# Performance work log

Hardware: AMD Instinct MI355X
Metric: run time of the kernel (lower is better)

The kernel has to match this reference:

```python
import jax, jax.numpy as jnp
import numpy as np

D_MODEL = 256
D_INNER = 512   # expand * d_model
NHEADS = 8
HEADDIM = 64    # d_inner // nheads
NGROUPS = 1
MDIST = 16


def setup_inputs() -> dict:
    key = jax.random.key(0)
    ks = jax.random.split(key, 12)
    B, L, Q = 4, 2048, 300
    in_key = jax.random.normal(ks[0], (B, L, D_MODEL), jnp.float32)
    in_query = jax.random.normal(ks[1], (B, Q, D_MODEL), jnp.float32)
    dist = jax.random.normal(ks[2], (B, L, Q, MDIST), jnp.float32)

    def lin(k, out_f, in_f):  # torch nn.Linear default init (kaiming-uniform-ish)
        bound = 1.0 / np.sqrt(in_f)
        return jax.random.uniform(k, (out_f, in_f), jnp.float32, -bound, bound)

    W_key = lin(ks[3], 2 * D_INNER + 2 * NGROUPS + NHEADS, D_MODEL)
    W_query = lin(ks[4], D_INNER, D_MODEL)
    W_bc = lin(ks[5], 2 * NGROUPS, MDIST)
    W_dt = lin(ks[6], NHEADS, MDIST)
    # dt_bias init (inverse-softplus of dt sampled log-uniform in [1e-4, 0.1])
    dt_min, dt_max = 1e-4, 0.1
    dtv = jnp.exp(jax.random.uniform(ks[7], (NHEADS,)) * (np.log(dt_max) - np.log(dt_min)) + np.log(dt_min))
    dtv = jnp.clip(dtv, 1e-4, None)
    dt_bias = dtv + jnp.log(-jnp.expm1(-dtv))
    A_log = jnp.log(jax.random.uniform(ks[8], (NHEADS,), minval=1.0, maxval=16.0))
    Dp = jnp.ones((NHEADS,), jnp.float32)
    W_out_key = lin(ks[9], D_MODEL, D_INNER)
    W_out_query = lin(ks[10], D_MODEL, D_INNER)
    key_norm_w = jnp.ones((D_INNER,), jnp.float32)
    ln_w = jnp.ones((D_INNER,), jnp.float32)
    ln_b = jnp.zeros((D_INNER,), jnp.float32)
    return dict(in_key=in_key, in_query=in_query, dist=dist, W_key=W_key, W_query=W_query,
                W_bc=W_bc, W_dt=W_dt, dt_bias=dt_bias, A_log=A_log, Dp=Dp,
                W_out_key=W_out_key, W_out_query=W_out_query, key_norm_w=key_norm_w,
                ln_w=ln_w, ln_b=ln_b)


def _issm_scan(x, S0, dt, A, Bm, Cm, Dp):
    """Selective scan with per-(l,h,n) dt and per-(l,n) B,C (ngroups=1).
    x: (B,L,H,P)  dt: (B,L,H,N)  Bm,Cm: (B,L,N)  S0: (B,H,P,N)  A: (H,)  Dp: (H,)
    """
    xs = (jnp.moveaxis(x, 1, 0), jnp.moveaxis(dt, 1, 0),
          jnp.moveaxis(Bm, 1, 0), jnp.moveaxis(Cm, 1, 0))

    def step(S, inp):
        xl, dtl, Bl, Cl = inp               # (B,H,P), (B,H,N), (B,N), (B,N)
        dA = jnp.exp(dtl * A[None, :, None])            # (B,H,N)
        dBx = (dtl * Bl[:, None, :])[:, :, None, :] * xl[:, :, :, None]
        S = S * dA[:, :, None, :] + dBx                 # (B,H,P,N)
        y = jnp.einsum('bhpn,bn->bhp', S, Cl) + Dp[None, :, None] * xl
        return S, y

    Sf, ys = jax.lax.scan(step, S0, xs)
    return jnp.moveaxis(ys, 0, 1), Sf       # (B,L,H,P), (B,H,P,N)


def reference(in_key, in_query, dist, W_key, W_query, W_bc, W_dt, dt_bias, A_log, Dp,
              W_out_key, W_out_query, key_norm_w, ln_w, ln_b):
    B, L, _ = in_key.shape
    Q = in_query.shape[1]
    zxbcdt = in_key @ W_key.T                            # (B,L,2*Din+2g+H)
    z = zxbcdt[..., :D_INNER]
    x = zxbcdt[..., D_INNER:2 * D_INNER].reshape(B, L, NHEADS, HEADDIM)
    b_bias = zxbcdt[..., 2 * D_INNER:2 * D_INNER + 1]    # (B,L,1)
    c_bias = zxbcdt[..., 2 * D_INNER + 1:2 * D_INNER + 2]
    dt_proj_bias = zxbcdt[..., 2 * D_INNER + 2:]         # (B,L,H)

    # initial state: (B,H,P,Q) -- state dim N == num_queries
    S0 = (in_query @ W_query.T).reshape(B, Q, NHEADS, HEADDIM).transpose(0, 2, 3, 1)
    A = -jnp.exp(A_log)                                  # (H,), constant over state dim

    bc = jnp.einsum('blqm,cm->blqc', dist, W_bc)         # (B,L,Q,2)
    Bm = bc[..., 0] + b_bias                             # (B,L,Q)
    Cm = bc[..., 1] + c_bias
    dtb = jnp.einsum('blqm,hm->blhq', dist, W_dt)        # (B,L,H,Q)
    dt = jax.nn.softplus(dtb + dt_proj_bias[..., None] + dt_bias[None, None, :, None])

    y_f, S_f = _issm_scan(x, S0, dt, A, Bm, Cm, Dp)
    # bidirectional: backward branch uses identical (cloned) x/B/C, flipped along L
    y_b, S_b = _issm_scan(x[:, ::-1], S0, dt[:, ::-1], A, Bm[:, ::-1], Cm[:, ::-1], Dp)
    y = (y_f + y_b[:, ::-1]) * 0.5
    S = (S_f + S_b) * 0.5

    key = y.reshape(B, L, D_INNER)
    g = key * jax.nn.silu(z)                             # gated RMSNorm, norm_before_gate=False
    key = g * jax.lax.rsqrt(jnp.mean(g * g, -1, keepdims=True) + 1e-5) * key_norm_w
    out_key = key @ W_out_key.T

    ls = S.transpose(0, 3, 1, 2).reshape(B, Q, D_INNER)  # b h p q -> b q (h p)
    mu = jnp.mean(ls, -1, keepdims=True)
    var = jnp.mean((ls - mu) ** 2, -1, keepdims=True)
    ls = (ls - mu) * jax.lax.rsqrt(var + 1e-5) * ln_w + ln_b
    out_query = ls @ W_out_query.T
    return out_key, out_query
```

## Files before the change

kernel.cpp:

```cpp
#include <hip/hip_runtime.h>
#include <hip/hip_bf16.h>

#define D_MODEL 256
#define D_INNER 512
#define NHEADS 8
#define HEADDIM 64
#define MDIST 16
#define BB 4
#define LL 2048
#define QQ 300
#define QP 320
#define NSEG 16
#define SEGLEN 128

typedef unsigned short ushort_t;
typedef __attribute__((ext_vector_type(8))) short bf16x8;
typedef __attribute__((ext_vector_type(4))) float f32x4;
typedef __attribute__((ext_vector_type(2))) float f32x2;

__device__ __forceinline__ void bf16_split(float v, ushort_t& hi, ushort_t& lo) {
    __hip_bfloat16 h = __float2bfloat16(v);
    float hf = __bfloat162float(h);
    __hip_bfloat16 l = __float2bfloat16(v - hf);
    hi = *(ushort_t*)&h;
    lo = *(ushort_t*)&l;
}

__device__ __forceinline__ f32x2 shfl_xor2(f32x2 v, int m) {
    f32x2 r;
    r.x = __shfl_xor(v.x, m, 64);
    r.y = __shfl_xor(v.y, m, 64);
    return r;
}

template<int CTRL>
__device__ __forceinline__ f32x2 dpp2(f32x2 v) {
    f32x2 r;
    r.x = __int_as_float(__builtin_amdgcn_update_dpp(0, __float_as_int(v.x), CTRL, 0xF, 0xF, true));
    r.y = __int_as_float(__builtin_amdgcn_update_dpp(0, __float_as_int(v.y), CTRL, 0xF, 0xF, true));
    return r;
}
template<int OFF>
__device__ __forceinline__ f32x2 swz2(f32x2 v) {
    f32x2 r;
    r.x = __int_as_float(__builtin_amdgcn_ds_swizzle(__float_as_int(v.x), OFF));
    r.y = __int_as_float(__builtin_amdgcn_ds_swizzle(__float_as_int(v.y), OFF));
    return r;
}

__global__ __launch_bounds__(256) void c_split(const float* __restrict__ in,
                                               ushort_t* __restrict__ hi,
                                               ushort_t* __restrict__ lo, int n) {
    int i = blockIdx.x * 256 + threadIdx.x;
    if (i >= n) return;
    ushort_t h, l;
    bf16_split(in[i], h, l);
    hi[i] = h;
    lo[i] = l;
}

__global__ __launch_bounds__(256) void gemm_bf16s(const ushort_t* __restrict__ Ah,
                                                  const ushort_t* __restrict__ Al,
                                                  const ushort_t* __restrict__ Bh,
                                                  const ushort_t* __restrict__ Bl,
                                                  float* __restrict__ C,
                                                  int M, int N, int K) {
    int w = threadIdx.x >> 6, lane = threadIdx.x & 63;
    int n0 = blockIdx.x * 64;
    int m0 = blockIdx.y * 128 + w * 32;
    int lm = lane & 15, lk = (lane >> 4) * 8;
    f32x4 acc[2][4];
#pragma unroll
    for (int i = 0; i < 2; i++)
#pragma unroll
        for (int j = 0; j < 4; j++) acc[i][j] = {0.f, 0.f, 0.f, 0.f};

    for (int k0 = 0; k0 < K; k0 += 32) {
        bf16x8 ah[2], al[2], bh[4], blo[4];
#pragma unroll
        for (int mf = 0; mf < 2; mf++) {
            int row = m0 + mf * 16 + lm;
            if (row >= M) row = M - 1;
            size_t off = (size_t)row * K + k0 + lk;
            ah[mf] = *(const bf16x8*)(Ah + off);
            al[mf] = *(const bf16x8*)(Al + off);
        }
#pragma unroll
        for (int nf = 0; nf < 4; nf++) {
            int col = n0 + nf * 16 + lm;
            size_t off = (size_t)col * K + k0 + lk;
            bh[nf]  = *(const bf16x8*)(Bh + off);
            blo[nf] = *(const bf16x8*)(Bl + off);
        }
#pragma unroll
        for (int mf = 0; mf < 2; mf++)
#pragma unroll
            for (int nf = 0; nf < 4; nf++) {
                acc[mf][nf] = __builtin_amdgcn_mfma_f32_16x16x32_bf16(ah[mf], bh[nf],  acc[mf][nf], 0, 0, 0);
                acc[mf][nf] = __builtin_amdgcn_mfma_f32_16x16x32_bf16(ah[mf], blo[nf], acc[mf][nf], 0, 0, 0);
                acc[mf][nf] = __builtin_amdgcn_mfma_f32_16x16x32_bf16(al[mf], bh[nf],  acc[mf][nf], 0, 0, 0);
            }
    }
#pragma unroll
    for (int mf = 0; mf < 2; mf++)
#pragma unroll
        for (int nf = 0; nf < 4; nf++)
#pragma unroll
            for (int r = 0; r < 4; r++) {
                int m = m0 + mf * 16 + (lane >> 4) * 4 + r;
                if (m < M) C[(size_t)m * N + n0 + nf * 16 + lm] = acc[mf][nf][r];
            }
}

__global__ __launch_bounds__(256) void k1b_bias(const float* __restrict__ in_key,
                                                const float* __restrict__ W_key,
                                                float* __restrict__ bias10) {
    int w = threadIdx.x >> 6, lane = threadIdx.x & 63;
    int row = blockIdx.x * 4 + w;
    float4 a = *(const float4*)(in_key + (size_t)row * 256 + lane * 4);
#pragma unroll
    for (int c = 0; c < 10; c++) {
        float4 b = *(const float4*)(W_key + (size_t)(1024 + c) * 256 + lane * 4);
        float t = a.x * b.x + a.y * b.y + a.z * b.z + a.w * b.w;
#pragma unroll
        for (int o = 32; o > 0; o >>= 1) t += __shfl_down(t, o, 64);
        if (lane == 0) bias10[row * 10 + c] = t;
    }
}

__global__ __launch_bounds__(256) void k2_dist(const float* __restrict__ dist,
                                               const float* __restrict__ bias10,
                                               const float* __restrict__ W_bc,
                                               const float* __restrict__ W_dt,
                                               const float* __restrict__ dt_bias,
                                               const float* __restrict__ A_log,
                                               float* __restrict__ dAB,
                                               float* __restrict__ Cm) {
    __shared__ float sWbc[32], sWdt[128], sb[8], sA[8];
    int tid = threadIdx.x;
    if (tid < 32) sWbc[tid] = W_bc[tid];
    else if (tid < 160) sWdt[tid - 32] = W_dt[tid - 32];
    else if (tid < 168) sb[tid - 160] = dt_bias[tid - 160];
    else if (tid < 176) sA[tid - 168] = -expf(A_log[tid - 168]);
    __syncthreads();
    int gid = blockIdx.x * 256 + tid;
    if (gid >= BB * LL * QQ) return;
    int q = gid % QQ;
    int bl = gid / QQ;
    const float* dp = dist + (size_t)gid * 16;
    float d[16];
    float4 d0 = *(const float4*)(dp + 0);
    float4 d1 = *(const float4*)(dp + 4);
    float4 d2 = *(const float4*)(dp + 8);
    float4 d3 = *(const float4*)(dp + 12);
    d[0]=d0.x; d[1]=d0.y; d[2]=d0.z; d[3]=d0.w;
    d[4]=d1.x; d[5]=d1.y; d[6]=d1.z; d[7]=d1.w;
    d[8]=d2.x; d[9]=d2.y; d[10]=d2.z; d[11]=d2.w;
    d[12]=d3.x; d[13]=d3.y; d[14]=d3.z; d[15]=d3.w;
    float bc0 = 0.f, bc1 = 0.f;
#pragma unroll
    for (int m = 0; m < 16; m++) {
        bc0 = fmaf(d[m], sWbc[m], bc0);
        bc1 = fmaf(d[m], sWbc[16 + m], bc1);
    }
    float Bmv = bc0 + bias10[bl * 10 + 0];
    float Cv  = bc1 + bias10[bl * 10 + 1];
    Cm[bl * QP + q] = Cv;
#pragma unroll
    for (int h = 0; h < 8; h++) {
        float t = 0.f;
#pragma unroll
        for (int m = 0; m < 16; m++) t = fmaf(d[m], sWdt[h * 16 + m], t);
        float pre = t + bias10[bl * 10 + 2 + h] + sb[h];
        float dt = (pre > 20.f) ? pre : log1pf(expf(pre));
        int o = (bl * 8 + h) * QP + q;
        float2 v;
        v.x = expf(sA[h] * dt);
        v.y = dt * Bmv;
        *(float2*)(dAB + (size_t)o * 2) = v;
    }
}

__global__ __launch_bounds__(256) void k2b_segdecay(const float* __restrict__ dAB,
                                                    float* __restrict__ segd) {
    int gid = blockIdx.x * 256 + threadIdx.x;
    if (gid >= BB * NSEG * 8 * QP) return;
    int q = gid % QP; int r = gid / QP;
    int h = r % 8; r /= 8;
    int s = r % NSEG; int b = r / NSEG;
    size_t base = (size_t)((b * LL + s * SEGLEN) * 8 + h) * QP + q;
    float p = 1.f;
    for (int i = 0; i < SEGLEN; i++) p *= dAB[(base + (size_t)i * 8 * QP) * 2];
    segd[gid] = p;
}

__global__ __launch_bounds__(256) void pass_ac(const float* __restrict__ dAB,
                                               const float* __restrict__ Cm,
                                               const float* __restrict__ zx,
                                               float* __restrict__ S_local,
                                               float* __restrict__ yf,
                                               float* __restrict__ yb) {
    __shared__ __align__(16) float sOp[2][4096];
    int seg = blockIdx.x, bh = blockIdx.y, dir = blockIdx.z;
    int tid = threadIdx.x;
    int w = tid >> 6, lane = tid & 63;
    int p0 = w * 16;
    int b = bh >> 3, h = bh & 7;
    f32x2 S2[40];
#pragma unroll
    for (int j = 0; j < 40; j++) S2[j] = {0.f, 0.f};
    float* __restrict__ yo = dir ? yb : yf;
    bool s1 = (lane & 1) != 0, s2b = (lane & 2) != 0, s4 = (lane & 4) != 0;

    int pos = tid * 4;
    auto stage = [&](int g, int buf) {
#pragma unroll
        for (int r = 0; r < 4; r++) {
            int i = g * 4 + r;
            int l = dir ? (LL - 1 - (seg * SEGLEN + i)) : (seg * SEGLEN + i);
            int bl = b * LL + l;
            const float* src;
            if (pos < 640)      src = dAB + (size_t)(bl * 8 + h) * 640 + pos;
            else if (pos < 960) src = Cm + (size_t)bl * QP + (pos - 640);
            else                src = zx + (size_t)bl * 1024 + 512 + h * 64 + (pos - 960);
            *(float4*)&sOp[buf][r * 1024 + pos] = *(const float4*)src;
        }
    };
    stage(0, 0);
    const int NGRP = SEGLEN / 4;
    for (int g = 0; g < NGRP; g++) {
        __syncthreads();
        if (g + 1 < NGRP) stage(g + 1, (g + 1) & 1);
        const float* bufg = &sOp[g & 1][0];
#pragma unroll
        for (int it = 0; it < 4; it++) {
            const float* Bq = bufg + it * 1024;
            float4 xq0 = *(const float4*)(Bq + 960 + p0);
            float4 xq1 = *(const float4*)(Bq + 964 + p0);
            float4 xq2 = *(const float4*)(Bq + 968 + p0);
            float4 xq3 = *(const float4*)(Bq + 972 + p0);
            f32x2 x2[8] = {{xq0.x, xq0.y}, {xq0.z, xq0.w}, {xq1.x, xq1.y}, {xq1.z, xq1.w},
                           {xq2.x, xq2.y}, {xq2.z, xq2.w}, {xq3.x, xq3.y}, {xq3.z, xq3.w}};
            f32x2 y[8];
#pragma unroll
            for (int j = 0; j < 8; j++) y[j] = {0.f, 0.f};
#pragma unroll
            for (int k = 0; k < 5; k++) {
                int n = k * 64 + lane;
                f32x2 ab = *(const f32x2*)(Bq + 2 * n);
                float c = Bq[640 + n];
                f32x2 a2 = {ab.x, ab.x}, b2 = {ab.y, ab.y}, c2 = {c, c};
#pragma unroll
                for (int j = 0; j < 8; j++) {
                    f32x2 s = S2[k * 8 + j] * a2 + b2 * x2[j];
                    S2[k * 8 + j] = s;
                    y[j] += s * c2;
                }
            }
            f32x2 u, v, z0, z1, z2, z3, w0, w1, q;
            u = s1 ? y[1] : y[0]; v = s1 ? y[0] : y[1]; z0 = u + dpp2<0xB1>(v);
            u = s1 ? y[3] : y[2]; v = s1 ? y[2] : y[3]; z1 = u + dpp2<0xB1>(v);
            u = s1 ? y[5] : y[4]; v = s1 ? y[4] : y[5]; z2 = u + dpp2<0xB1>(v);
            u = s1 ? y[7] : y[6]; v = s1 ? y[6] : y[7]; z3 = u + dpp2<0xB1>(v);
            u = s2b ? z1 : z0; v = s2b ? z0 : z1; w0 = u + dpp2<0x4E>(v);
            u = s2b ? z3 : z2; v = s2b ? z2 : z3; w1 = u + dpp2<0x4E>(v);
            u = s4 ? w1 : w0; v = s4 ? w0 : w1; q = u + swz2<0x101F>(v);
            q = q + dpp2<0x128>(q);
            q = q + swz2<0x401F>(q);
            q = q + shfl_xor2(q, 32);
            if (lane < 8) {
                int i = g * 4 + it;
                int l = dir ? (LL - 1 - (seg * SEGLEN + i)) : (seg * SEGLEN + i);
                int bl = b * LL + l;
                *(f32x2*)(yo + (size_t)(bl * 8 + h) * 64 + p0 + 2 * lane) = q;
            }
        }
    }
    size_t base = (size_t)((dir * NSEG + seg) * 32 + bh) * QP * 64;
#pragma unroll
    for (int k = 0; k < 5; k++) {
        int n = k * 64 + lane;
#pragma unroll
        for (int t = 0; t < 4; t++) {
            float4 vv = {S2[k * 8 + 2 * t].x, S2[k * 8 + 2 * t].y,
                         S2[k * 8 + 2 * t + 1].x, S2[k * 8 + 2 * t + 1].y};
            *(float4*)&S_local[base + (size_t)n * 64 + p0 + 4 * t] = vv;
        }
    }
}

__global__ __launch_bounds__(256) void pass_b(const float* __restrict__ S_local,
                                              const float* __restrict__ segd,
                                              const float* __restrict__ S0q,
                                              float* __restrict__ S_in,
                                              float* __restrict__ Savg) {
    int gid = blockIdx.x * 256 + threadIdx.x;
    if (gid >= BB * 8 * QP * 64) return;
    int p = gid & 63; int r = gid >> 6;
    int n = r % QP; r /= QP;
    int h = r & 7; int b = r >> 3;
    int bh = b * 8 + h;
    float s0 = (n < QQ) ? S0q[(size_t)(b * QQ + n) * 512 + h * 64 + p] : 0.f;
    float Sf = 0.f, Sb = 0.f;
    for (int dir = 0; dir < 2; dir++) {
        float S = s0;
        for (int s = 0; s < NSEG; s++) {
            size_t idx = (size_t)(((dir * NSEG + s) * 32 + bh) * QP + n) * 64 + p;
            S_in[idx] = S;
            int sf = dir ? (NSEG - 1 - s) : s;
            float dec = segd[((b * NSEG + sf) * 8 + h) * QP + n];
            S = fmaf(S, dec, S_local[idx]);
        }
        if (dir == 0) Sf = S; else Sb = S;
    }
    Savg[((bh) * QP + n) * 64 + p] = 0.5f * (Sf + Sb);
}

__global__ __launch_bounds__(256) void k3_corr(const float* __restrict__ dAB,
                                               const float* __restrict__ Cm,
                                               const float* __restrict__ Sin,
                                               float* __restrict__ yf,
                                               float* __restrict__ yb) {
    __shared__ __align__(16) ushort_t sAh[128][48], sAl[128][48];
    __shared__ __align__(16) ushort_t sBh[64][48], sBl[64][48];
    __shared__ float pref[8][32];
    int seg = blockIdx.x, bh = blockIdx.y, dir = blockIdx.z;
    int b = bh >> 3, h = bh & 7;
    int tid = threadIdx.x;
    int w = tid >> 6, lane = tid & 63;
    int lm = lane & 15, lkq = lane >> 4;
    f32x4 acc[2][4];
#pragma unroll
    for (int i = 0; i < 2; i++)
#pragma unroll
        for (int j = 0; j < 4; j++) acc[i][j] = {0.f, 0.f, 0.f, 0.f};
    size_t sinBase = (size_t)((dir * NSEG + seg) * 32 + bh) * QP * 64;
    int nl = tid & 31, iseg = tid >> 5;

    for (int k0 = 0; k0 < QP; k0 += 32) {
        __syncthreads();
#pragma unroll
        for (int r = 0; r < 8; r++) {
            int flat = tid + r * 256;
            int kn = flat >> 6, p = flat & 63;
            float v = Sin[sinBase + (size_t)(k0 + kn) * 64 + p];
            ushort_t hi, lo;
            bf16_split(v, hi, lo);
            sBh[p][kn] = hi;
            sBl[p][kn] = lo;
        }
        float da[16], cm[16];
#pragma unroll
        for (int k = 0; k < 16; k++) {
            int i = iseg * 16 + k;
            int l = dir ? (LL - 1 - (seg * SEGLEN + i)) : (seg * SEGLEN + i);
            int bl = b * LL + l;
            da[k] = dAB[((size_t)(bl * 8 + h) * QP + k0 + nl) * 2];
            cm[k] = Cm[(size_t)bl * QP + k0 + nl];
        }
        float lp = 1.f;
#pragma unroll
        for (int k = 0; k < 16; k++) lp *= da[k];
        pref[iseg][nl] = lp;
        __syncthreads();
        if (tid < 32) {
            float c = 1.f;
#pragma unroll
            for (int s = 0; s < 8; s++) {
                float t = pref[s][tid];
                pref[s][tid] = c;
                c *= t;
            }
        }
        __syncthreads();
        float cum = pref[iseg][nl];
#pragma unroll
        for (int k = 0; k < 16; k++) {
            cum *= da[k];
            float v = cum * cm[k];
            ushort_t hi, lo;
            bf16_split(v, hi, lo);
            int i = iseg * 16 + k;
            sAh[i][nl] = hi;
            sAl[i][nl] = lo;
        }
        __syncthreads();
        bf16x8 ah[2], al[2], bhf[4], blf[4];
#pragma unroll
        for (int mf = 0; mf < 2; mf++) {
            int row = w * 32 + mf * 16 + lm;
            ah[mf] = *(const bf16x8*)&sAh[row][lkq * 8];
            al[mf] = *(const bf16x8*)&sAl[row][lkq * 8];
        }
#pragma unroll
        for (int nf = 0; nf < 4; nf++) {
            int p = nf * 16 + lm;
            bhf[nf] = *(const bf16x8*)&sBh[p][lkq * 8];
            blf[nf] = *(const bf16x8*)&sBl[p][lkq * 8];
        }
#pragma unroll
        for (int mf = 0; mf < 2; mf++)
#pragma unroll
            for (int nf = 0; nf < 4; nf++) {
                acc[mf][nf] = __builtin_amdgcn_mfma_f32_16x16x32_bf16(ah[mf], bhf[nf], acc[mf][nf], 0, 0, 0);
                acc[mf][nf] = __builtin_amdgcn_mfma_f32_16x16x32_bf16(ah[mf], blf[nf], acc[mf][nf], 0, 0, 0);
                acc[mf][nf] = __builtin_amdgcn_mfma_f32_16x16x32_bf16(al[mf], bhf[nf], acc[mf][nf], 0, 0, 0);
            }
    }
    float* __restrict__ yo = dir ? yb : yf;
#pragma unroll
    for (int mf = 0; mf < 2; mf++)
#pragma unroll
        for (int nf = 0; nf < 4; nf++)
#pragma unroll
            for (int r = 0; r < 4; r++) {
                int i = w * 32 + mf * 16 + lkq * 4 + r;
                int p = nf * 16 + lm;
                int l = dir ? (LL - 1 - (seg * SEGLEN + i)) : (seg * SEGLEN + i);
                size_t idx = (size_t)((b * LL + l) * 8 + h) * 64 + p;
                yo[idx] += acc[mf][nf][r];
            }
}

__global__ __launch_bounds__(512) void k4_gate(const float* __restrict__ yf,
                                               const float* __restrict__ yb,
                                               const float* __restrict__ zx,
                                               const float* __restrict__ Dp,
                                               const float* __restrict__ knw,
                                               ushort_t* __restrict__ kh,
                                               ushort_t* __restrict__ kl) {
    int bl = blockIdx.x;
    int t = threadIdx.x;
    int h = t >> 6;
    float x = zx[(size_t)bl * 1024 + 512 + t];
    float yv = 0.5f * (yf[(size_t)bl * 512 + t] + yb[(size_t)bl * 512 + t]) + Dp[h] * x;
    float z = zx[(size_t)bl * 1024 + t];
    float g = yv * (z / (1.f + expf(-z)));
    float v = g * g;
#pragma unroll
    for (int o = 32; o > 0; o >>= 1) v += __shfl_down(v, o, 64);
    __shared__ float rs[8];
    __shared__ float stot;
    if ((t & 63) == 0) rs[t >> 6] = v;
    __syncthreads();
    if (t == 0) {
        float s = 0.f;
#pragma unroll
        for (int i = 0; i < 8; i++) s += rs[i];
        stot = s;
    }
    __syncthreads();
    float rms = rsqrtf(stot / 512.f + 1e-5f);
    float kv = g * rms * knw[t];
    ushort_t hi, lo;
    bf16_split(kv, hi, lo);
    kh[(size_t)bl * 512 + t] = hi;
    kl[(size_t)bl * 512 + t] = lo;
}

__global__ __launch_bounds__(512) void k5_ln(const float* __restrict__ Savg,
                                             const float* __restrict__ lnw,
                                             const float* __restrict__ lnb,
                                             ushort_t* __restrict__ lh,
                                             ushort_t* __restrict__ ll) {
    int bq = blockIdx.x;
    int b = bq / QQ, q = bq % QQ;
    int t = threadIdx.x;
    int h = t >> 6, p = t & 63;
    float v = Savg[((b * 8 + h) * QP + q) * 64 + p];
    float s1 = v, s2 = v * v;
#pragma unroll
    for (int o = 32; o > 0; o >>= 1) {
        s1 += __shfl_down(s1, o, 64);
        s2 += __shfl_down(s2, o, 64);
    }
    __shared__ float r1[8], r2[8];
    __shared__ float smu, srv;
    if ((t & 63) == 0) { r1[t >> 6] = s1; r2[t >> 6] = s2; }
    __syncthreads();
    if (t == 0) {
        float a = 0.f, c = 0.f;
#pragma unroll
        for (int i = 0; i < 8; i++) { a += r1[i]; c += r2[i]; }
        float mu = a / 512.f;
        float var = c / 512.f - mu * mu;
        smu = mu;
        srv = rsqrtf(var + 1e-5f);
    }
    __syncthreads();
    float ov = (v - smu) * srv * lnw[t] + lnb[t];
    ushort_t hi, lo;
    bf16_split(ov, hi, lo);
    lh[(size_t)bq * 512 + t] = hi;
    ll[(size_t)bq * 512 + t] = lo;
}

extern "C" void kernel_launch(void* const* d_in, const int* in_sizes, int n_in,
                              void* d_out, int out_size, void* d_ws, size_t ws_size,
                              hipStream_t stream) {
    const float* in_key    = (const float*)d_in[0];
    const float* in_query  = (const float*)d_in[1];
    const float* dist      = (const float*)d_in[2];
    const float* W_key     = (const float*)d_in[3];
    const float* W_query   = (const float*)d_in[4];
    const float* W_bc      = (const float*)d_in[5];
    const float* W_dt      = (const float*)d_in[6];
    const float* dt_bias   = (const float*)d_in[7];
    const float* A_log     = (const float*)d_in[8];
    const float* Dp        = (const float*)d_in[9];
    const float* W_out_key = (const float*)d_in[10];
    const float* W_out_query = (const float*)d_in[11];
    const float* key_norm_w = (const float*)d_in[12];
    const float* ln_w      = (const float*)d_in[13];
    const float* ln_b      = (const float*)d_in[14];

    float* out_key = (float*)d_out;
    float* out_query = out_key + (size_t)BB * LL * D_MODEL;

    char* w8 = (char*)d_ws;
    auto alloc = [&](size_t bytes) {
        char* ptr = w8;
        w8 += (bytes + 255) & ~(size_t)255;
        return ptr;
    };
    float* zx     = (float*)alloc((size_t)8192 * 1024 * 4);
    float* bias10 = (float*)alloc((size_t)8192 * 10 * 4);
    float* S0q    = (float*)alloc((size_t)1200 * 512 * 4);
    float* dABb   = (float*)alloc((size_t)8192 * 8 * QP * 2 * 4);
    float* Cmb    = (float*)alloc((size_t)8192 * QP * 4);
    float* segd   = (float*)alloc((size_t)BB * NSEG * 8 * QP * 4);
    float* Sloc   = (float*)alloc((size_t)2 * NSEG * 32 * QP * 64 * 4);
    float* Sin    = (float*)alloc((size_t)2 * NSEG * 32 * QP * 64 * 4);
    float* yfb    = (float*)alloc((size_t)8192 * 512 * 4);
    float* ybb    = (float*)alloc((size_t)8192 * 512 * 4);
    float* Savg   = (float*)alloc((size_t)32 * QP * 64 * 4);
    ushort_t* ink_h  = (ushort_t*)alloc((size_t)2097152 * 2);
    ushort_t* ink_l  = (ushort_t*)alloc((size_t)2097152 * 2);
    ushort_t* wk_h   = (ushort_t*)alloc((size_t)262144 * 2);
    ushort_t* wk_l   = (ushort_t*)alloc((size_t)262144 * 2);
    ushort_t* inq_h  = (ushort_t*)alloc((size_t)307200 * 2);
    ushort_t* inq_l  = (ushort_t*)alloc((size_t)307200 * 2);
    ushort_t* wq_h   = (ushort_t*)alloc((size_t)131072 * 2);
    ushort_t* wq_l   = (ushort_t*)alloc((size_t)131072 * 2);
    ushort_t* keyb_h = (ushort_t*)alloc((size_t)4194304 * 2);
    ushort_t* keyb_l = (ushort_t*)alloc((size_t)4194304 * 2);
    ushort_t* wok_h  = (ushort_t*)alloc((size_t)131072 * 2);
    ushort_t* wok_l  = (ushort_t*)alloc((size_t)131072 * 2);
    ushort_t* lsn_h  = (ushort_t*)alloc((size_t)614400 * 2);
    ushort_t* lsn_l  = (ushort_t*)alloc((size_t)614400 * 2);
    ushort_t* woq_h  = (ushort_t*)alloc((size_t)131072 * 2);
    ushort_t* woq_l  = (ushort_t*)alloc((size_t)131072 * 2);

    c_split<<<8192, 256, 0, stream>>>(in_key, ink_h, ink_l, 2097152);
    c_split<<<1024, 256, 0, stream>>>(W_key, wk_h, wk_l, 262144);
    c_split<<<1200, 256, 0, stream>>>(in_query, inq_h, inq_l, 307200);
    c_split<<<512, 256, 0, stream>>>(W_query, wq_h, wq_l, 131072);
    c_split<<<512, 256, 0, stream>>>(W_out_key, wok_h, wok_l, 131072);
    c_split<<<512, 256, 0, stream>>>(W_out_query, woq_h, woq_l, 131072);

    gemm_bf16s<<<dim3(16, 64), 256, 0, stream>>>(ink_h, ink_l, wk_h, wk_l, zx, 8192, 1024, 256);
    k1b_bias<<<2048, 256, 0, stream>>>(in_key, W_key, bias10);
    gemm_bf16s<<<dim3(8, 10), 256, 0, stream>>>(inq_h, inq_l, wq_h, wq_l, S0q, 1200, 512, 256);

    k2_dist<<<9600, 256, 0, stream>>>(dist, bias10, W_bc, W_dt, dt_bias, A_log, dABb, Cmb);
    k2b_segdecay<<<640, 256, 0, stream>>>(dABb, segd);

    pass_ac<<<dim3(NSEG, 32, 2), 256, 0, stream>>>(dABb, Cmb, zx, Sloc, yfb, ybb);
    pass_b<<<2560, 256, 0, stream>>>(Sloc, segd, S0q, Sin, Savg);
    k3_corr<<<dim3(NSEG, 32, 2), 256, 0, stream>>>(dABb, Cmb, Sin, yfb, ybb);

    k4_gate<<<8192, 512, 0, stream>>>(yfb, ybb, zx, Dp, key_norm_w, keyb_h, keyb_l);
    gemm_bf16s<<<dim3(4, 64), 256, 0, stream>>>(keyb_h, keyb_l, wok_h, wok_l, out_key, 8192, 256, 512);

    k5_ln<<<1200, 512, 0, stream>>>(Savg, ln_w, ln_b, lsn_h, lsn_l);
    gemm_bf16s<<<dim3(4, 10), 256, 0, stream>>>(lsn_h, lsn_l, woq_h, woq_l, out_query, 1200, 256, 512);
}
```

Measured before the change: 907.5 us.

## Split scan pass across P halves, register-prefetch operands, fuse segment decay

The chunked scan kernel now splits each head's 64 P columns across two blocks, which doubles the grid and halves per-thread state registers. Shared-memory double buffering and barriers are replaced with direct global loads into a register double buffer. The separate segment-decay kernel is removed, and its product of dA is accumulated inside the scan and written by one wave. Explicit packed FMA/MUL asm is used for the state update. The trade-off is that each block re-reads dA, B and C, so those loads are duplicated across the two P-halves.

```diff
diff --git a/kernel.cpp b/kernel.cpp
--- a/kernel.cpp
+++ b/kernel.cpp
@@ -46,6 +46,17 @@
     r.x = __int_as_float(__builtin_amdgcn_ds_swizzle(__float_as_int(v.x), OFF));
     r.y = __int_as_float(__builtin_amdgcn_ds_swizzle(__float_as_int(v.y), OFF));
     return r;
+}
+
+__device__ __forceinline__ f32x2 pk_mul(f32x2 a, f32x2 b) {
+    f32x2 d;
+    asm("v_pk_mul_f32 %0, %1, %2" : "=v"(d) : "v"(a), "v"(b));
+    return d;
+}
+__device__ __forceinline__ f32x2 pk_fma(f32x2 a, f32x2 b, f32x2 c) {
+    f32x2 d;
+    asm("v_pk_fma_f32 %0, %1, %2, %3" : "=v"(d) : "v"(a), "v"(b), "v"(c));
+    return d;
 }
 
 __global__ __launch_bounds__(256) void c_split(const float* __restrict__ in,
@@ -181,111 +192,98 @@
     }
 }
 
-__global__ __launch_bounds__(256) void k2b_segdecay(const float* __restrict__ dAB,
-                                                    float* __restrict__ segd) {
-    int gid = blockIdx.x * 256 + threadIdx.x;
-    if (gid >= BB * NSEG * 8 * QP) return;
-    int q = gid % QP; int r = gid / QP;
-    int h = r % 8; r /= 8;
-    int s = r % NSEG; int b = r / NSEG;
-    size_t base = (size_t)((b * LL + s * SEGLEN) * 8 + h) * QP + q;
-    float p = 1.f;
-    for (int i = 0; i < SEGLEN; i++) p *= dAB[(base + (size_t)i * 8 * QP) * 2];
-    segd[gid] = p;
-}
-
 __global__ __launch_bounds__(256) void pass_ac(const float* __restrict__ dAB,
                                                const float* __restrict__ Cm,
                                                const float* __restrict__ zx,
                                                float* __restrict__ S_local,
+                                               float* __restrict__ segd,
                                                float* __restrict__ yf,
                                                float* __restrict__ yb) {
-    __shared__ __align__(16) float sOp[2][4096];
-    int seg = blockIdx.x, bh = blockIdx.y, dir = blockIdx.z;
+    int seg = blockIdx.x >> 1, ph = blockIdx.x & 1;
+    int bh = blockIdx.y, dir = blockIdx.z;
     int tid = threadIdx.x;
     int w = tid >> 6, lane = tid & 63;
-    int p0 = w * 16;
+    int p0 = ph * 32 + w * 8;
     int b = bh >> 3, h = bh & 7;
-    f32x2 S2[40];
-#pragma unroll
-    for (int j = 0; j < 40; j++) S2[j] = {0.f, 0.f};
+    f32x2 S2[20];
+#pragma unroll
+    for (int j = 0; j < 20; j++) S2[j] = {0.f, 0.f};
+    float prodA[5];
+#pragma unroll
+    for (int k = 0; k < 5; k++) prodA[k] = 1.f;
     float* __restrict__ yo = dir ? yb : yf;
-    bool s1 = (lane & 1) != 0, s2b = (lane & 2) != 0, s4 = (lane & 4) != 0;
-
-    int pos = tid * 4;
-    auto stage = [&](int g, int buf) {
-#pragma unroll
-        for (int r = 0; r < 4; r++) {
-            int i = g * 4 + r;
+    bool s1 = (lane & 1) != 0, s2b = (lane & 2) != 0;
+
+    auto LD = [&](int i, f32x2 (&AB)[5], float (&C)[5], float4 (&X)[2]) {
+        int l = dir ? (LL - 1 - (seg * SEGLEN + i)) : (seg * SEGLEN + i);
+        int bl = b * LL + l;
+        const float* pa = dAB + (size_t)(bl * 8 + h) * (QP * 2);
+        const float* pc = Cm + (size_t)bl * QP;
+        const float* px = zx + (size_t)bl * 1024 + 512 + h * 64 + p0;
+#pragma unroll
+        for (int k = 0; k < 5; k++) {
+            AB[k] = *(const f32x2*)(pa + 2 * (k * 64 + lane));
+            C[k] = pc[k * 64 + lane];
+        }
+        X[0] = *(const float4*)(px);
+        X[1] = *(const float4*)(px + 4);
+    };
+
+    auto STEP = [&](int i, f32x2 (&AB)[5], float (&C)[5], float4 (&X)[2]) {
+        f32x2 x2[4] = {{X[0].x, X[0].y}, {X[0].z, X[0].w},
+                       {X[1].x, X[1].y}, {X[1].z, X[1].w}};
+        f32x2 y0 = {0.f, 0.f}, y1 = {0.f, 0.f}, y2v = {0.f, 0.f}, y3 = {0.f, 0.f};
+#pragma unroll
+        for (int k = 0; k < 5; k++) {
+            f32x2 a2 = {AB[k].x, AB[k].x};
+            f32x2 b2 = {AB[k].y, AB[k].y};
+            f32x2 c2 = {C[k], C[k]};
+            prodA[k] *= AB[k].x;
+            f32x2 t, s;
+            t = pk_mul(b2, x2[0]); s = pk_fma(S2[k * 4 + 0], a2, t); S2[k * 4 + 0] = s; y0  = pk_fma(s, c2, y0);
+            t = pk_mul(b2, x2[1]); s = pk_fma(S2[k * 4 + 1], a2, t); S2[k * 4 + 1] = s; y1  = pk_fma(s, c2, y1);
+            t = pk_mul(b2, x2[2]); s = pk_fma(S2[k * 4 + 2], a2, t); S2[k * 4 + 2] = s; y2v = pk_fma(s, c2, y2v);
+            t = pk_mul(b2, x2[3]); s = pk_fma(S2[k * 4 + 3], a2, t); S2[k * 4 + 3] = s; y3  = pk_fma(s, c2, y3);
+        }
+        f32x2 u, v, z0, z1, q;
+        u = s1 ? y1 : y0;  v = s1 ? y0 : y1;   z0 = u + dpp2<0xB1>(v);
+        u = s1 ? y3 : y2v; v = s1 ? y2v : y3;  z1 = u + dpp2<0xB1>(v);
+        u = s2b ? z1 : z0; v = s2b ? z0 : z1;  q = u + dpp2<0x4E>(v);
+        q = q + swz2<0x101F>(q);
+        q = q + dpp2<0x128>(q);
+        q = q + swz2<0x401F>(q);
+        q = q + shfl_xor2(q, 32);
+        if (lane < 4) {
             int l = dir ? (LL - 1 - (seg * SEGLEN + i)) : (seg * SEGLEN + i);
             int bl = b * LL + l;
-            const float* src;
-            if (pos < 640)      src = dAB + (size_t)(bl * 8 + h) * 640 + pos;
-            else if (pos < 960) src = Cm + (size_t)bl * QP + (pos - 640);
-            else                src = zx + (size_t)bl * 1024 + 512 + h * 64 + (pos - 960);
-            *(float4*)&sOp[buf][r * 1024 + pos] = *(const float4*)src;
+            *(f32x2*)(yo + (size_t)(bl * 8 + h) * 64 + p0 + 2 * lane) = q;
         }
     };
-    stage(0, 0);
-    const int NGRP = SEGLEN / 4;
-    for (int g = 0; g < NGRP; g++) {
-        __syncthreads();
-        if (g + 1 < NGRP) stage(g + 1, (g + 1) & 1);
-        const float* bufg = &sOp[g & 1][0];
-#pragma unroll
-        for (int it = 0; it < 4; it++) {
-            const float* Bq = bufg + it * 1024;
-            float4 xq0 = *(const float4*)(Bq + 960 + p0);
-            float4 xq1 = *(const float4*)(Bq + 964 + p0);
-            float4 xq2 = *(const float4*)(Bq + 968 + p0);
-            float4 xq3 = *(const float4*)(Bq + 972 + p0);
-            f32x2 x2[8] = {{xq0.x, xq0.y}, {xq0.z, xq0.w}, {xq1.x, xq1.y}, {xq1.z, xq1.w},
-                           {xq2.x, xq2.y}, {xq2.z, xq2.w}, {xq3.x, xq3.y}, {xq3.z, xq3.w}};
-            f32x2 y[8];
-#pragma unroll
-            for (int j = 0; j < 8; j++) y[j] = {0.f, 0.f};
-#pragma unroll
-            for (int k = 0; k < 5; k++) {
-                int n = k * 64 + lane;
-                f32x2 ab = *(const f32x2*)(Bq + 2 * n);
-                float c = Bq[640 + n];
-                f32x2 a2 = {ab.x, ab.x}, b2 = {ab.y, ab.y}, c2 = {c, c};
-#pragma unroll
-                for (int j = 0; j < 8; j++) {
-                    f32x2 s = S2[k * 8 + j] * a2 + b2 * x2[j];
-                    S2[k * 8 + j] = s;
-                    y[j] += s * c2;
-                }
-            }
-            f32x2 u, v, z0, z1, z2, z3, w0, w1, q;
-            u = s1 ? y[1] : y[0]; v = s1 ? y[0] : y[1]; z0 = u + dpp2<0xB1>(v);
-            u = s1 ? y[3] : y[2]; v = s1 ? y[2] : y[3]; z1 = u + dpp2<0xB1>(v);
-            u = s1 ? y[5] : y[4]; v = s1 ? y[4] : y[5]; z2 = u + dpp2<0xB1>(v);
-            u = s1 ? y[7] : y[6]; v = s1 ? y[6] : y[7]; z3 = u + dpp2<0xB1>(v);
-            u = s2b ? z1 : z0; v = s2b ? z0 : z1; w0 = u + dpp2<0x4E>(v);
-            u = s2b ? z3 : z2; v = s2b ? z2 : z3; w1 = u + dpp2<0x4E>(v);
-            u = s4 ? w1 : w0; v = s4 ? w0 : w1; q = u + swz2<0x101F>(v);
-            q = q + dpp2<0x128>(q);
-            q = q + swz2<0x401F>(q);
-            q = q + shfl_xor2(q, 32);
-            if (lane < 8) {
-                int i = g * 4 + it;
-                int l = dir ? (LL - 1 - (seg * SEGLEN + i)) : (seg * SEGLEN + i);
-                int bl = b * LL + l;
-                *(f32x2*)(yo + (size_t)(bl * 8 + h) * 64 + p0 + 2 * lane) = q;
-            }
-        }
+
+    f32x2 abA[5], abB[5];
+    float cA[5], cB[5];
+    float4 xA[2], xB[2];
+    LD(0, abA, cA, xA);
+#pragma unroll 1
+    for (int i = 0; i < SEGLEN; i += 2) {
+        LD(i + 1, abB, cB, xB);
+        STEP(i, abA, cA, xA);
+        if (i + 2 < SEGLEN) LD(i + 2, abA, cA, xA);
+        STEP(i + 1, abB, cB, xB);
     }
     size_t base = (size_t)((dir * NSEG + seg) * 32 + bh) * QP * 64;
 #pragma unroll
     for (int k = 0; k < 5; k++) {
         int n = k * 64 + lane;
-#pragma unroll
-        for (int t = 0; t < 4; t++) {
-            float4 vv = {S2[k * 8 + 2 * t].x, S2[k * 8 + 2 * t].y,
-                         S2[k * 8 + 2 * t + 1].x, S2[k * 8 + 2 * t + 1].y};
-            *(float4*)&S_local[base + (size_t)n * 64 + p0 + 4 * t] = vv;
-        }
+        float4 v0 = {S2[k * 4 + 0].x, S2[k * 4 + 0].y, S2[k * 4 + 1].x, S2[k * 4 + 1].y};
+        float4 v1 = {S2[k * 4 + 2].x, S2[k * 4 + 2].y, S2[k * 4 + 3].x, S2[k * 4 + 3].y};
+        *(float4*)&S_local[base + (size_t)n * 64 + p0] = v0;
+        *(float4*)&S_local[base + (size_t)n * 64 + p0 + 4] = v1;
+    }
+    if (dir == 0 && ph == 0 && w == 0) {
+#pragma unroll
+        for (int k = 0; k < 5; k++)
+            segd[((b * NSEG + seg) * 8 + h) * QP + k * 64 + lane] = prodA[k];
     }
 }
 
@@ -563,9 +561,8 @@
     gemm_bf16s<<<dim3(8, 10), 256, 0, stream>>>(inq_h, inq_l, wq_h, wq_l, S0q, 1200, 512, 256);
 
     k2_dist<<<9600, 256, 0, stream>>>(dist, bias10, W_bc, W_dt, dt_bias, A_log, dABb, Cmb);
-    k2b_segdecay<<<640, 256, 0, stream>>>(dABb, segd);
-
-    pass_ac<<<dim3(NSEG, 32, 2), 256, 0, stream>>>(dABb, Cmb, zx, Sloc, yfb, ybb);
+
+    pass_ac<<<dim3(NSEG * 2, 32, 2), 256, 0, stream>>>(dABb, Cmb, zx, Sloc, segd, yfb, ybb);
     pass_b<<<2560, 256, 0, stream>>>(Sloc, segd, S0q, Sin, Savg);
     k3_corr<<<dim3(NSEG, 32, 2), 256, 0, stream>>>(dABb, Cmb, Sin, yfb, ybb);
 
```

New measurement: 977.6 us. 1.08x slower.
